# Performance work log

Hardware: AMD Instinct MI355X
Metric: run time of the kernel (lower is better)

The kernel has to match this reference:

```python
import jax, jax.numpy as jnp
import numpy as np

B, S, D = 2, 2048, 1024      # batch, seq, d_model
H, DH = 16, 64               # heads, head_dim
E, F, K = 16, 256, 2         # n_experts, expert_size, top_k


def setup_inputs() -> dict:
    key = jax.random.key(0)
    ks = jax.random.split(key, 12)
    w = lambda k, shape: (jax.random.normal(k, shape, jnp.float32) * 0.02)
    return {
        "hidden_states": jax.random.normal(ks[0], (B, S, D), jnp.float32),
        "Wq": w(ks[1], (D, D)),
        "Wk": w(ks[2], (D, D)),
        "Wv": w(ks[3], (D, D)),
        "Wo": w(ks[4], (D, D)),
        "ln1_scale": jnp.ones((D,), jnp.float32),
        "ln1_bias": jnp.zeros((D,), jnp.float32),
        "ln2_scale": jnp.ones((D,), jnp.float32),
        "ln2_bias": jnp.zeros((D,), jnp.float32),
        "W_sel": w(ks[5], (D, E)),
        "W1": w(ks[6], (E, D, F)),
        "W2": w(ks[7], (E, F, D)),
    }


def _layernorm(x, scale, bias, eps=1e-5):
    mu = jnp.mean(x, axis=-1, keepdims=True)
    var = jnp.mean(jnp.square(x - mu), axis=-1, keepdims=True)
    return (x - mu) * jax.lax.rsqrt(var + eps) * scale + bias


def reference(hidden_states, Wq, Wk, Wv, Wo, ln1_scale, ln1_bias,
              ln2_scale, ln2_bias, W_sel, W1, W2):
    x = hidden_states
    # ---- self-attention sublayer (pre-LN, residual) ----
    h = _layernorm(x, ln1_scale, ln1_bias)
    q = (h @ Wq).reshape(B, S, H, DH)
    k = (h @ Wk).reshape(B, S, H, DH)
    v = (h @ Wv).reshape(B, S, H, DH)
    scores = jnp.einsum("bqhd,bkhd->bhqk", q, k) / np.float32(np.sqrt(DH))
    attn = jax.nn.softmax(scores, axis=-1)
    ctx = jnp.einsum("bhqk,bkhd->bqhd", attn, v).reshape(B, S, D)
    x = x + ctx @ Wo

    # ---- SigmaMoE FFN sublayer (pre-LN, residual) ----
    h = _layernorm(x, ln2_scale, ln2_bias).reshape(B * S, D)  # [T, D]
    sel = jax.nn.sigmoid(h @ W_sel)                            # [T, E]
    vals, idx = jax.lax.top_k(sel, K)                          # [T, K]
    T = B * S
    gates = jnp.zeros((T, E), h.dtype).at[jnp.arange(T)[:, None], idx].set(vals)
    # expert MLPs, gate applied to each expert's output
    up = jax.nn.relu(jnp.einsum("td,edf->tef", h, W1))         # [T, E, F]
    up = up * gates[:, :, None]
    moe_out = jnp.einsum("tef,efd->td", up, W2).reshape(B, S, D)
    return x + moe_out
```

## Files before the change

kernel.cpp:

```cpp
#include <hip/hip_runtime.h>

typedef unsigned short u16;
typedef __attribute__((ext_vector_type(8))) short s16x8;
typedef __attribute__((ext_vector_type(4))) float f32x4;

typedef __attribute__((address_space(3))) unsigned int lds_u32_t;
typedef __attribute__((address_space(1))) unsigned int glb_u32_t;

__device__ __forceinline__ float bf2f(u16 u) {
    union { unsigned int i; float f; } c; c.i = ((unsigned int)u) << 16; return c.f;
}
__device__ __forceinline__ u16 f2bf(float f) {
    union { float f; unsigned int u; } c; c.f = f;
    unsigned int u = c.u;
    unsigned int r = (u + 0x7fffu + ((u >> 16) & 1u)) >> 16;
    return (u16)r;
}
__device__ __forceinline__ void glds16(const u16* g, short* l) {
    __builtin_amdgcn_global_load_lds((glb_u32_t*)g, (lds_u32_t*)l, 16, 0, 0);
}

__global__ __launch_bounds__(256) void transpose_split_kernel(const float* __restrict__ src,
                                                              u16* __restrict__ dh,
                                                              u16* __restrict__ dl,
                                                              int R, int C) {
    __shared__ float tile[32][33];
    int c0 = blockIdx.x * 32, r0 = blockIdx.y * 32;
    int tx = threadIdx.x & 31, ty = threadIdx.x >> 5;
    for (int i = 0; i < 4; i++)
        tile[ty + 8 * i][tx] = src[(size_t)(r0 + ty + 8 * i) * C + c0 + tx];
    __syncthreads();
    for (int i = 0; i < 4; i++) {
        float v = tile[tx][ty + 8 * i];
        u16 hb = f2bf(v);
        size_t idx = (size_t)(c0 + ty + 8 * i) * R + r0 + tx;
        dh[idx] = hb;
        dl[idx] = f2bf(v - bf2f(hb));
    }
}

__global__ __launch_bounds__(256) void transpose_f2b_kernel(const float* __restrict__ src,
                                                            u16* __restrict__ dst,
                                                            int R, int C) {
    __shared__ float tile[32][33];
    size_t zoff = (size_t)blockIdx.z * R * C;
    int c0 = blockIdx.x * 32, r0 = blockIdx.y * 32;
    int tx = threadIdx.x & 31, ty = threadIdx.x >> 5;
    for (int i = 0; i < 4; i++)
        tile[ty + 8 * i][tx] = src[zoff + (size_t)(r0 + ty + 8 * i) * C + c0 + tx];
    __syncthreads();
    for (int i = 0; i < 4; i++)
        dst[zoff + (size_t)(c0 + ty + 8 * i) * R + r0 + tx] = f2bf(tile[tx][ty + 8 * i]);
}

__global__ __launch_bounds__(256) void ln_split_kernel(const float* __restrict__ x,
                                                       const float* __restrict__ sc,
                                                       const float* __restrict__ bi,
                                                       u16* __restrict__ oh,
                                                       u16* __restrict__ ol) {
    int row = blockIdx.x, tid = threadIdx.x;
    f32x4 u = *(const f32x4*)(x + (size_t)row * 1024 + tid * 4);
    float s = u[0] + u[1] + u[2] + u[3];
    float ss = u[0]*u[0] + u[1]*u[1] + u[2]*u[2] + u[3]*u[3];
    for (int off = 1; off < 64; off <<= 1) { s += __shfl_xor(s, off, 64); ss += __shfl_xor(ss, off, 64); }
    __shared__ float red[8];
    if ((tid & 63) == 0) { red[tid >> 6] = s; red[4 + (tid >> 6)] = ss; }
    __syncthreads();
    s = red[0] + red[1] + red[2] + red[3];
    ss = red[4] + red[5] + red[6] + red[7];
    float mu = s * (1.0f / 1024.0f);
    float rstd = rsqrtf(ss * (1.0f / 1024.0f) - mu * mu + 1e-5f);
    f32x4 g = *(const f32x4*)(sc + tid * 4);
    f32x4 b = *(const f32x4*)(bi + tid * 4);
    size_t o = (size_t)row * 1024 + tid * 4;
    for (int i = 0; i < 4; i++) {
        float v = (u[i] - mu) * rstd * g[i] + b[i];
        u16 hb = f2bf(v);
        oh[o + i] = hb;
        ol[o + i] = f2bf(v - bf2f(hb));
    }
}

__global__ __launch_bounds__(256) void ln_f2b_kernel(const float* __restrict__ x,
                                                     const float* __restrict__ sc,
                                                     const float* __restrict__ bi,
                                                     u16* __restrict__ out) {
    int row = blockIdx.x, tid = threadIdx.x;
    f32x4 u = *(const f32x4*)(x + (size_t)row * 1024 + tid * 4);
    float s = u[0] + u[1] + u[2] + u[3];
    float ss = u[0]*u[0] + u[1]*u[1] + u[2]*u[2] + u[3]*u[3];
    for (int off = 1; off < 64; off <<= 1) { s += __shfl_xor(s, off, 64); ss += __shfl_xor(ss, off, 64); }
    __shared__ float red[8];
    if ((tid & 63) == 0) { red[tid >> 6] = s; red[4 + (tid >> 6)] = ss; }
    __syncthreads();
    s = red[0] + red[1] + red[2] + red[3];
    ss = red[4] + red[5] + red[6] + red[7];
    float mu = s * (1.0f / 1024.0f);
    float rstd = rsqrtf(ss * (1.0f / 1024.0f) - mu * mu + 1e-5f);
    f32x4 g = *(const f32x4*)(sc + tid * 4);
    f32x4 b = *(const f32x4*)(bi + tid * 4);
    u16* op = out + (size_t)row * 1024 + tid * 4;
    for (int i = 0; i < 4; i++)
        op[i] = f2bf((u[i] - mu) * rstd * g[i] + b[i]);
}

__global__ __launch_bounds__(256) void gemm3_qkv(const u16* __restrict__ Ah_g,
                                                 const u16* __restrict__ Al_g,
                                                 const u16* __restrict__ Bh_g,
                                                 const u16* __restrict__ Bl_g,
                                                 u16* __restrict__ Ch, u16* __restrict__ Cl,
                                                 float scale) {
    const int K = 1024;
    __shared__ __align__(16) short Ahs[128 * 32], Als[128 * 32];
    __shared__ __align__(16) short Bhs[128 * 32], Bls[128 * 32];
    int m0 = blockIdx.y * 128, n0 = blockIdx.x * 128;
    int tid = threadIdx.x, lane = tid & 63, w = tid >> 6;
    int wm = (w & 1) * 64, wn = (w >> 1) * 64;
    int lr = lane & 15, lq = lane >> 4;
    int r0 = w * 32 + (lane >> 2);
    int cv = (lane & 3) * 8;
    const u16* pAh = Ah_g + (size_t)(m0 + r0) * K + cv;
    const u16* pAl = Al_g + (size_t)(m0 + r0) * K + cv;
    const u16* pBh = Bh_g + (size_t)(n0 + r0) * K + cv;
    const u16* pBl = Bl_g + (size_t)(n0 + r0) * K + cv;
    size_t st16 = (size_t)16 * K;
    f32x4 acc[4][4] = {};

    for (int k0 = 0; k0 < K; k0 += 32) {
        glds16(pAh + k0, &Ahs[w * 1024]);  glds16(pAh + k0 + st16, &Ahs[w * 1024 + 512]);
        glds16(pAl + k0, &Als[w * 1024]);  glds16(pAl + k0 + st16, &Als[w * 1024 + 512]);
        glds16(pBh + k0, &Bhs[w * 1024]);  glds16(pBh + k0 + st16, &Bhs[w * 1024 + 512]);
        glds16(pBl + k0, &Bls[w * 1024]);  glds16(pBl + k0 + st16, &Bls[w * 1024 + 512]);
        __syncthreads();
        s16x8 ah[4], al[4], bh[4], bl[4];
        #pragma unroll
        for (int i = 0; i < 4; i++) {
            int off = (wm + i * 16 + lr) * 32 + lq * 8;
            ah[i] = *(const s16x8*)&Ahs[off];
            al[i] = *(const s16x8*)&Als[off];
        }
        #pragma unroll
        for (int j = 0; j < 4; j++) {
            int off = (wn + j * 16 + lr) * 32 + lq * 8;
            bh[j] = *(const s16x8*)&Bhs[off];
            bl[j] = *(const s16x8*)&Bls[off];
        }
        #pragma unroll
        for (int i = 0; i < 4; i++)
            #pragma unroll
            for (int j = 0; j < 4; j++) {
                acc[i][j] = __builtin_amdgcn_mfma_f32_16x16x32_bf16(al[i], bh[j], acc[i][j], 0, 0, 0);
                acc[i][j] = __builtin_amdgcn_mfma_f32_16x16x32_bf16(ah[i], bl[j], acc[i][j], 0, 0, 0);
                acc[i][j] = __builtin_amdgcn_mfma_f32_16x16x32_bf16(ah[i], bh[j], acc[i][j], 0, 0, 0);
            }
        __syncthreads();
    }

    int seg = n0 >> 10;
    float sc = (seg == 0) ? scale : 1.0f;
    u16* Chp = Ch + (size_t)seg * 8388608;
    u16* Clp = Cl + (size_t)seg * 8388608;
    int c0 = (n0 & 1023) + wn;
    #pragma unroll
    for (int i = 0; i < 4; i++)
        #pragma unroll
        for (int j = 0; j < 4; j++)
            #pragma unroll
            for (int r = 0; r < 4; r++) {
                int row = m0 + wm + i * 16 + lq * 4 + r;
                int col = c0 + j * 16 + lr;
                float vv = acc[i][j][r] * sc;
                u16 hb = f2bf(vv);
                u16 lb = f2bf(vv - bf2f(hb));
                size_t idx = (size_t)row * 1024 + col;
                Chp[idx] = hb; Clp[idx] = lb;
            }
}

__global__ __launch_bounds__(256) void gemm3_res(const u16* __restrict__ Ah_g,
                                                 const u16* __restrict__ Al_g,
                                                 const u16* __restrict__ Bh_g,
                                                 const u16* __restrict__ Bl_g,
                                                 float* __restrict__ C,
                                                 const float* __restrict__ res) {
    const int K = 1024, N = 1024;
    __shared__ __align__(16) short Ahs[128 * 32], Als[128 * 32];
    __shared__ __align__(16) short Bhs[128 * 32], Bls[128 * 32];
    int m0 = blockIdx.y * 128, n0 = blockIdx.x * 128;
    int tid = threadIdx.x, lane = tid & 63, w = tid >> 6;
    int wm = (w & 1) * 64, wn = (w >> 1) * 64;
    int lr = lane & 15, lq = lane >> 4;
    int r0 = w * 32 + (lane >> 2);
    int cv = (lane & 3) * 8;
    const u16* pAh = Ah_g + (size_t)(m0 + r0) * K + cv;
    const u16* pAl = Al_g + (size_t)(m0 + r0) * K + cv;
    const u16* pBh = Bh_g + (size_t)(n0 + r0) * K + cv;
    const u16* pBl = Bl_g + (size_t)(n0 + r0) * K + cv;
    size_t st16 = (size_t)16 * K;
    f32x4 acc[4][4] = {};

    for (int k0 = 0; k0 < K; k0 += 32) {
        glds16(pAh + k0, &Ahs[w * 1024]);  glds16(pAh + k0 + st16, &Ahs[w * 1024 + 512]);
        glds16(pAl + k0, &Als[w * 1024]);  glds16(pAl + k0 + st16, &Als[w * 1024 + 512]);
        glds16(pBh + k0, &Bhs[w * 1024]);  glds16(pBh + k0 + st16, &Bhs[w * 1024 + 512]);
        glds16(pBl + k0, &Bls[w * 1024]);  glds16(pBl + k0 + st16, &Bls[w * 1024 + 512]);
        __syncthreads();
        s16x8 ah[4], al[4], bh[4], bl[4];
        #pragma unroll
        for (int i = 0; i < 4; i++) {
            int off = (wm + i * 16 + lr) * 32 + lq * 8;
            ah[i] = *(const s16x8*)&Ahs[off];
            al[i] = *(const s16x8*)&Als[off];
        }
        #pragma unroll
        for (int j = 0; j < 4; j++) {
            int off = (wn + j * 16 + lr) * 32 + lq * 8;
            bh[j] = *(const s16x8*)&Bhs[off];
            bl[j] = *(const s16x8*)&Bls[off];
        }
        #pragma unroll
        for (int i = 0; i < 4; i++)
            #pragma unroll
            for (int j = 0; j < 4; j++) {
                acc[i][j] = __builtin_amdgcn_mfma_f32_16x16x32_bf16(al[i], bh[j], acc[i][j], 0, 0, 0);
                acc[i][j] = __builtin_amdgcn_mfma_f32_16x16x32_bf16(ah[i], bl[j], acc[i][j], 0, 0, 0);
                acc[i][j] = __builtin_amdgcn_mfma_f32_16x16x32_bf16(ah[i], bh[j], acc[i][j], 0, 0, 0);
            }
        __syncthreads();
    }

    #pragma unroll
    for (int i = 0; i < 4; i++)
        #pragma unroll
        for (int j = 0; j < 4; j++)
            #pragma unroll
            for (int r = 0; r < 4; r++) {
                int row = m0 + wm + i * 16 + lq * 4 + r;
                int col = n0 + wn + j * 16 + lr;
                size_t idx = (size_t)row * N + col;
                C[idx] = acc[i][j][r] + res[idx];
            }
}

__global__ __launch_bounds__(256) void gemm_moe_up(const u16* __restrict__ A,
                                                   const u16* __restrict__ BT,
                                                   u16* __restrict__ C,
                                                   const float* __restrict__ gates) {
    const int K = 1024, N = 4096;
    __shared__ __align__(16) short As[128 * 32];
    __shared__ __align__(16) short Bs[128 * 32];
    int m0 = blockIdx.y * 128, n0 = blockIdx.x * 128;
    int tid = threadIdx.x, lane = tid & 63, w = tid >> 6;
    int wm = (w & 1) * 64, wn = (w >> 1) * 64;
    int lr = lane & 15, lq = lane >> 4;
    int r0 = w * 32 + (lane >> 2);
    int cv = (lane & 3) * 8;
    const u16* pA = A  + (size_t)(m0 + r0) * K + cv;
    const u16* pB = BT + (size_t)(n0 + r0) * K + cv;
    size_t st16 = (size_t)16 * K;
    f32x4 acc[4][4] = {};

    for (int k0 = 0; k0 < K; k0 += 32) {
        glds16(pA + k0, &As[w * 1024]);  glds16(pA + k0 + st16, &As[w * 1024 + 512]);
        glds16(pB + k0, &Bs[w * 1024]);  glds16(pB + k0 + st16, &Bs[w * 1024 + 512]);
        __syncthreads();
        s16x8 av[4], bv[4];
        #pragma unroll
        for (int i = 0; i < 4; i++) av[i] = *(const s16x8*)&As[(wm + i * 16 + lr) * 32 + lq * 8];
        #pragma unroll
        for (int j = 0; j < 4; j++) bv[j] = *(const s16x8*)&Bs[(wn + j * 16 + lr) * 32 + lq * 8];
        #pragma unroll
        for (int i = 0; i < 4; i++)
            #pragma unroll
            for (int j = 0; j < 4; j++)
                acc[i][j] = __builtin_amdgcn_mfma_f32_16x16x32_bf16(av[i], bv[j], acc[i][j], 0, 0, 0);
        __syncthreads();
    }

    #pragma unroll
    for (int i = 0; i < 4; i++)
        #pragma unroll
        for (int j = 0; j < 4; j++)
            #pragma unroll
            for (int r = 0; r < 4; r++) {
                int row = m0 + wm + i * 16 + lq * 4 + r;
                int col = n0 + wn + j * 16 + lr;
                float g = gates[(size_t)row * 16 + (col >> 8)];
                C[(size_t)row * N + col] = f2bf(fmaxf(acc[i][j][r], 0.0f) * g);
            }
}

__global__ __launch_bounds__(256) void gemm_moe_down(const u16* __restrict__ A,
                                                     const u16* __restrict__ BT,
                                                     float* __restrict__ C,
                                                     const float* __restrict__ res) {
    const int K = 4096, N = 1024;
    __shared__ __align__(16) short As[128 * 32];
    __shared__ __align__(16) short Bs[128 * 32];
    int m0 = blockIdx.y * 128, n0 = blockIdx.x * 128;
    int tid = threadIdx.x, lane = tid & 63, w = tid >> 6;
    int wm = (w & 1) * 64, wn = (w >> 1) * 64;
    int lr = lane & 15, lq = lane >> 4;
    int r0 = w * 32 + (lane >> 2);
    int cv = (lane & 3) * 8;
    const u16* pA = A  + (size_t)(m0 + r0) * K + cv;
    const u16* pB = BT + (size_t)(n0 + r0) * K + cv;
    size_t st16 = (size_t)16 * K;
    f32x4 acc[4][4] = {};

    for (int k0 = 0; k0 < K; k0 += 32) {
        glds16(pA + k0, &As[w * 1024]);  glds16(pA + k0 + st16, &As[w * 1024 + 512]);
        glds16(pB + k0, &Bs[w * 1024]);  glds16(pB + k0 + st16, &Bs[w * 1024 + 512]);
        __syncthreads();
        s16x8 av[4], bv[4];
        #pragma unroll
        for (int i = 0; i < 4; i++) av[i] = *(const s16x8*)&As[(wm + i * 16 + lr) * 32 + lq * 8];
        #pragma unroll
        for (int j = 0; j < 4; j++) bv[j] = *(const s16x8*)&Bs[(wn + j * 16 + lr) * 32 + lq * 8];
        #pragma unroll
        for (int i = 0; i < 4; i++)
            #pragma unroll
            for (int j = 0; j < 4; j++)
                acc[i][j] = __builtin_amdgcn_mfma_f32_16x16x32_bf16(av[i], bv[j], acc[i][j], 0, 0, 0);
        __syncthreads();
    }

    #pragma unroll
    for (int i = 0; i < 4; i++)
        #pragma unroll
        for (int j = 0; j < 4; j++)
            #pragma unroll
            for (int r = 0; r < 4; r++) {
                int row = m0 + wm + i * 16 + lq * 4 + r;
                int col = n0 + wn + j * 16 + lr;
                size_t idx = (size_t)row * N + col;
                C[idx] = acc[i][j][r] + res[idx];
            }
}

__global__ __launch_bounds__(256) void vtrans_kernel(const u16* __restrict__ v_hi,
                                                     const u16* __restrict__ v_lo,
                                                     u16* __restrict__ vT_hi,
                                                     u16* __restrict__ vT_lo) {
    __shared__ __align__(16) short tile[64][72];
    int st = blockIdx.x, bh = blockIdx.y;
    int b = bh >> 4, h = bh & 15;
    int tid = threadIdx.x;
    int i = tid >> 2, seg = (tid & 3) * 16;
    for (int p = 0; p < 2; p++) {
        const u16* src = p ? v_lo : v_hi;
        u16* dst = p ? vT_lo : vT_hi;
        size_t goff = (size_t)(b * 2048 + st * 64 + i) * 1024 + h * 64 + seg;
        *(s16x8*)&tile[i][seg]     = *(const s16x8*)&src[goff];
        *(s16x8*)&tile[i][seg + 8] = *(const s16x8*)&src[goff + 8];
        __syncthreads();
        s16x8 o0, o1;
        for (int j = 0; j < 8; j++) { o0[j] = tile[seg + j][i]; o1[j] = tile[seg + 8 + j][i]; }
        size_t doff = ((size_t)bh * 64 + i) * 2048 + st * 64 + seg;
        *(s16x8*)&dst[doff]     = o0;
        *(s16x8*)&dst[doff + 8] = o1;
        __syncthreads();
    }
}

__global__ __launch_bounds__(256) void attn_mfma(const u16* __restrict__ qh_g,
                                                 const u16* __restrict__ ql_g,
                                                 const u16* __restrict__ kh_g,
                                                 const u16* __restrict__ kl_g,
                                                 const u16* __restrict__ vth_g,
                                                 const u16* __restrict__ vtl_g,
                                                 u16* __restrict__ ch_g,
                                                 u16* __restrict__ cl_g) {
    __shared__ __align__(16) short Ksh[64][72], Ksl[64][72], Vsh[64][72], Vsl[64][72];
    __shared__ __align__(16) short Ph[4][16 * 64], Pl[4][16 * 64];
    int lin = blockIdx.x + 16 * blockIdx.y;
    int xcd = lin & 7, rest = lin >> 3;
    int qt = rest & 15;
    int bh = xcd + 8 * (rest >> 4);
    int b = bh >> 4, h = bh & 15;
    int tid = threadIdx.x, w = tid >> 6, lane = tid & 63;
    int lr = lane & 15, lq = lane >> 4;
    int qbase = qt * 128 + w * 32;

    s16x8 qfh[2][2], qfl[2][2];
    for (int rt = 0; rt < 2; rt++)
        for (int kc = 0; kc < 2; kc++) {
            size_t qoff = (size_t)(b * 2048 + qbase + rt * 16 + lr) * 1024 + h * 64 + kc * 32 + lq * 8;
            qfh[rt][kc] = *(const s16x8*)&qh_g[qoff];
            qfl[rt][kc] = *(const s16x8*)&ql_g[qoff];
        }

    float m_[2][4], l_[2][4];
    f32x4 O[2][4] = {};
    for (int rt = 0; rt < 2; rt++)
        for (int r = 0; r < 4; r++) { m_[rt][r] = -1e30f; l_[rt][r] = 0.0f; }

    for (int kc0 = 0; kc0 < 2048; kc0 += 64) {
        {
            int kk = tid >> 2, seg = (tid & 3) * 16;
            size_t goff = (size_t)(b * 2048 + kc0 + kk) * 1024 + h * 64 + seg;
            *(s16x8*)&Ksh[kk][seg]     = *(const s16x8*)&kh_g[goff];
            *(s16x8*)&Ksh[kk][seg + 8] = *(const s16x8*)&kh_g[goff + 8];
            *(s16x8*)&Ksl[kk][seg]     = *(const s16x8*)&kl_g[goff];
            *(s16x8*)&Ksl[kk][seg + 8] = *(const s16x8*)&kl_g[goff + 8];
            size_t voff = ((size_t)bh * 64 + kk) * 2048 + kc0 + seg;
            *(s16x8*)&Vsh[kk][seg]     = *(const s16x8*)&vth_g[voff];
            *(s16x8*)&Vsh[kk][seg + 8] = *(const s16x8*)&vth_g[voff + 8];
            *(s16x8*)&Vsl[kk][seg]     = *(const s16x8*)&vtl_g[voff];
            *(s16x8*)&Vsl[kk][seg + 8] = *(const s16x8*)&vtl_g[voff + 8];
        }
        __syncthreads();

        f32x4 s[2][4] = {};
        for (int ct = 0; ct < 4; ct++)
            for (int kc = 0; kc < 2; kc++) {
                s16x8 kbh = *(const s16x8*)&Ksh[ct * 16 + lr][kc * 32 + lq * 8];
                s16x8 kbl = *(const s16x8*)&Ksl[ct * 16 + lr][kc * 32 + lq * 8];
                for (int rt = 0; rt < 2; rt++) {
                    s[rt][ct] = __builtin_amdgcn_mfma_f32_16x16x32_bf16(qfl[rt][kc], kbh, s[rt][ct], 0, 0, 0);
                    s[rt][ct] = __builtin_amdgcn_mfma_f32_16x16x32_bf16(qfh[rt][kc], kbl, s[rt][ct], 0, 0, 0);
                    s[rt][ct] = __builtin_amdgcn_mfma_f32_16x16x32_bf16(qfh[rt][kc], kbh, s[rt][ct], 0, 0, 0);
                }
            }

        for (int rt = 0; rt < 2; rt++) {
            float al[4];
            for (int ri = 0; ri < 4; ri++) {
                float mx = fmaxf(fmaxf(s[rt][0][ri], s[rt][1][ri]), fmaxf(s[rt][2][ri], s[rt][3][ri]));
                for (int off = 1; off < 16; off <<= 1) mx = fmaxf(mx, __shfl_xor(mx, off, 64));
                float mn = fmaxf(m_[rt][ri], mx);
                float a = __expf(m_[rt][ri] - mn);
                m_[rt][ri] = mn; al[ri] = a;
                float ps = 0.0f;
                for (int ct = 0; ct < 4; ct++) {
                    float p = __expf(s[rt][ct][ri] - mn);
                    s[rt][ct][ri] = p; ps += p;
                }
                for (int off = 1; off < 16; off <<= 1) ps += __shfl_xor(ps, off, 64);
                l_[rt][ri] = l_[rt][ri] * a + ps;
            }
            for (int nt = 0; nt < 4; nt++)
                for (int ri = 0; ri < 4; ri++) O[rt][nt][ri] *= al[ri];
            for (int ct = 0; ct < 4; ct++)
                for (int ri = 0; ri < 4; ri++) {
                    float p = s[rt][ct][ri];
                    u16 hb = f2bf(p);
                    u16 lb = f2bf(p - bf2f(hb));
                    int row = lq * 4 + ri, col = ct * 16 + lr;
                    int pidx = (row * 64 + col) ^ ((row & 7) << 3);
                    Ph[w][pidx] = (short)hb;
                    Pl[w][pidx] = (short)lb;
                }
            asm volatile("s_waitcnt lgkmcnt(0)" ::: "memory");
            __builtin_amdgcn_sched_barrier(0);
            __builtin_amdgcn_s_setprio(1);
            for (int kc = 0; kc < 2; kc++) {
                int pidx = (lr * 64 + kc * 32 + lq * 8) ^ ((lr & 7) << 3);
                s16x8 pah = *(const s16x8*)&Ph[w][pidx];
                s16x8 pal = *(const s16x8*)&Pl[w][pidx];
                for (int nt = 0; nt < 4; nt++) {
                    s16x8 vbh = *(const s16x8*)&Vsh[nt * 16 + lr][kc * 32 + lq * 8];
                    s16x8 vbl = *(const s16x8*)&Vsl[nt * 16 + lr][kc * 32 + lq * 8];
                    O[rt][nt] = __builtin_amdgcn_mfma_f32_16x16x32_bf16(pal, vbh, O[rt][nt], 0, 0, 0);
                    O[rt][nt] = __builtin_amdgcn_mfma_f32_16x16x32_bf16(pah, vbl, O[rt][nt], 0, 0, 0);
                    O[rt][nt] = __builtin_amdgcn_mfma_f32_16x16x32_bf16(pah, vbh, O[rt][nt], 0, 0, 0);
                }
            }
            __builtin_amdgcn_s_setprio(0);
            asm volatile("s_waitcnt lgkmcnt(0)" ::: "memory");
            __builtin_amdgcn_sched_barrier(0);
        }
        __syncthreads();
    }

    for (int rt = 0; rt < 2; rt++)
        for (int nt = 0; nt < 4; nt++)
            for (int ri = 0; ri < 4; ri++) {
                int row = qbase + rt * 16 + lq * 4 + ri;
                int d = nt * 16 + lr;
                float v = O[rt][nt][ri] / l_[rt][ri];
                u16 hb = f2bf(v);
                size_t idx = (size_t)(b * 2048 + row) * 1024 + h * 64 + d;
                ch_g[idx] = hb;
                cl_g[idx] = f2bf(v - bf2f(hb));
            }
}

__global__ __launch_bounds__(256) void router_kernel(const float* __restrict__ x2,
                                                     const float* __restrict__ sc,
                                                     const float* __restrict__ bi,
                                                     const float* __restrict__ Wsel,
                                                     float* __restrict__ gates) {
    int tid = threadIdx.x, w = tid >> 6, lane = tid & 63;
    int t = blockIdx.x * 4 + w;
    const float* xp = x2 + (size_t)t * 1024;
    float s = 0.0f, ss = 0.0f;
    for (int i = 0; i < 16; i++) {
        float v = xp[lane * 16 + i];
        s += v; ss += v * v;
    }
    for (int off = 1; off < 64; off <<= 1) { s += __shfl_xor(s, off, 64); ss += __shfl_xor(ss, off, 64); }
    float mu = s * (1.0f / 1024.0f);
    float rstd = rsqrtf(ss * (1.0f / 1024.0f) - mu * mu + 1e-5f);
    int e = lane & 15, part = lane >> 4;
    float acc = 0.0f;
    for (int d = part * 256; d < part * 256 + 256; d++) {
        float h = (xp[d] - mu) * rstd * sc[d] + bi[d];
        acc += h * Wsel[(size_t)d * 16 + e];
    }
    acc += __shfl_xor(acc, 16, 64);
    acc += __shfl_xor(acc, 32, 64);
    float v = 1.0f / (1.0f + __expf(-acc));
    float m1 = v;
    for (int off = 1; off < 64; off <<= 1) m1 = fmaxf(m1, __shfl_xor(m1, off, 64));
    unsigned long long b1 = __ballot(v == m1);
    int e1 = (__ffsll(b1) - 1) & 15;
    float v2 = (e == e1) ? -1e30f : v;
    float m2 = v2;
    for (int off = 1; off < 64; off <<= 1) m2 = fmaxf(m2, __shfl_xor(m2, off, 64));
    unsigned long long b2 = __ballot(v2 == m2);
    int e2 = (__ffsll(b2) - 1) & 15;
    if (lane < 16)
        gates[(size_t)t * 16 + e] = (e == e1) ? m1 : (e == e2 ? m2 : 0.0f);
}

extern "C" void kernel_launch(void* const* d_in, const int* in_sizes, int n_in,
                              void* d_out, int out_size, void* d_ws, size_t ws_size,
                              hipStream_t stream) {
    const float* x    = (const float*)d_in[0];
    const float* Wq   = (const float*)d_in[1];
    const float* Wk   = (const float*)d_in[2];
    const float* Wv   = (const float*)d_in[3];
    const float* Wo   = (const float*)d_in[4];
    const float* ln1s = (const float*)d_in[5];
    const float* ln1b = (const float*)d_in[6];
    const float* ln2s = (const float*)d_in[7];
    const float* ln2b = (const float*)d_in[8];
    const float* Wsel = (const float*)d_in[9];
    const float* W1   = (const float*)d_in[10];
    const float* W2   = (const float*)d_in[11];
    float* out = (float*)d_out;

    char* ws = (char*)d_ws;
    const size_t MB = 1024 * 1024;
    u16*   h1_h  = (u16*)  (ws + 0 * MB);
    u16*   h1_l  = (u16*)  (ws + 8 * MB);
    u16*   vT_hi = (u16*)  (ws + 0 * MB);
    u16*   vT_lo = (u16*)  (ws + 8 * MB);
    u16*   h2    = (u16*)  (ws + 0 * MB);
    float* gates = (float*)(ws + 8 * MB);
    u16*   q_hi  = (u16*)  (ws + 16 * MB);
    u16*   q_lo  = (u16*)  (ws + 24 * MB);
    u16*   k_hi  = (u16*)  (ws + 32 * MB);
    u16*   k_lo  = (u16*)  (ws + 40 * MB);
    u16*   up    = (u16*)  (ws + 16 * MB);
    u16*   v_hi  = (u16*)  (ws + 48 * MB);
    u16*   v_lo  = (u16*)  (ws + 56 * MB);
    u16*   ctx_h = (u16*)  (ws + 48 * MB);
    u16*   ctx_l = (u16*)  (ws + 56 * MB);
    float* x2    = (float*)(ws + 64 * MB);
    u16*   WqT_h = (u16*)  (ws + 80 * MB);
    u16*   WkT_h = (u16*)  (ws + 82 * MB);
    u16*   WvT_h = (u16*)  (ws + 84 * MB);
    u16*   WqT_l = (u16*)  (ws + 86 * MB);
    u16*   WkT_l = (u16*)  (ws + 88 * MB);
    u16*   WvT_l = (u16*)  (ws + 90 * MB);
    u16*   WoT_h = (u16*)  (ws + 92 * MB);
    u16*   WoT_l = (u16*)  (ws + 94 * MB);
    u16*   W1T   = (u16*)  (ws + 80 * MB);
    u16*   W2T   = (u16*)  (ws + 88 * MB);

    transpose_split_kernel<<<dim3(32, 32), 256, 0, stream>>>(Wq, WqT_h, WqT_l, 1024, 1024);
    transpose_split_kernel<<<dim3(32, 32), 256, 0, stream>>>(Wk, WkT_h, WkT_l, 1024, 1024);
    transpose_split_kernel<<<dim3(32, 32), 256, 0, stream>>>(Wv, WvT_h, WvT_l, 1024, 1024);
    transpose_split_kernel<<<dim3(32, 32), 256, 0, stream>>>(Wo, WoT_h, WoT_l, 1024, 1024);

    ln_split_kernel<<<4096, 256, 0, stream>>>(x, ln1s, ln1b, h1_h, h1_l);
    gemm3_qkv<<<dim3(24, 32), 256, 0, stream>>>(h1_h, h1_l, WqT_h, WqT_l, q_hi, q_lo, 0.125f);
    vtrans_kernel<<<dim3(32, 32), 256, 0, stream>>>(v_hi, v_lo, vT_hi, vT_lo);
    attn_mfma<<<dim3(16, 32), 256, 0, stream>>>(q_hi, q_lo, k_hi, k_lo, vT_hi, vT_lo, ctx_h, ctx_l);
    gemm3_res<<<dim3(8, 32), 256, 0, stream>>>(ctx_h, ctx_l, WoT_h, WoT_l, x2, x);
    ln_f2b_kernel<<<4096, 256, 0, stream>>>(x2, ln2s, ln2b, h2);
    router_kernel<<<1024, 256, 0, stream>>>(x2, ln2s, ln2b, Wsel, gates);
    transpose_f2b_kernel<<<dim3(8, 32, 16), 256, 0, stream>>>(W1, W1T, 1024, 256);
    transpose_f2b_kernel<<<dim3(32, 128, 1), 256, 0, stream>>>(W2, W2T, 4096, 1024);
    gemm_moe_up<<<dim3(32, 32), 256, 0, stream>>>(h2, W1T, up, gates);
    gemm_moe_down<<<dim3(8, 32), 256, 0, stream>>>(up, W2T, out, x2);
}
```

Measured before the change: 638.7 us.

## Route MoE tokens to experts and compute only selected expert GEMMs

The router now builds per-expert token lists with atomic counters. The up and down GEMMs gather only the tokens routed to each expert instead of running dense over all 16 experts. The down projection scatter-adds into the output with float atomics after an init kernel copies in the residual. This removes about 8x of the MoE FLOPs, but output summation order becomes nondeterministic and the grid assumes at most 80 row tiles.

```diff
diff --git a/kernel.cpp b/kernel.cpp
--- a/kernel.cpp
+++ b/kernel.cpp
@@ -242,27 +242,50 @@
             }
 }
 
-__global__ __launch_bounds__(256) void gemm_moe_up(const u16* __restrict__ A,
-                                                   const u16* __restrict__ BT,
-                                                   u16* __restrict__ C,
-                                                   const float* __restrict__ gates) {
-    const int K = 1024, N = 4096;
+__global__ __launch_bounds__(256) void init_out_kernel(const float* __restrict__ x2,
+                                                       float* __restrict__ out) {
+    size_t i = ((size_t)blockIdx.x * 256 + threadIdx.x) * 4;
+    *(f32x4*)(out + i) = *(const f32x4*)(x2 + i);
+}
+
+__global__ __launch_bounds__(256) void gemm_moe_up_sparse(const u16* __restrict__ h2,
+                                                          const u16* __restrict__ W1T,
+                                                          const int* __restrict__ cnt,
+                                                          const int* __restrict__ list,
+                                                          const float* __restrict__ gates,
+                                                          u16* __restrict__ up_buf) {
+    const int K = 1024;
     __shared__ __align__(16) short As[128 * 32];
     __shared__ __align__(16) short Bs[128 * 32];
-    int m0 = blockIdx.y * 128, n0 = blockIdx.x * 128;
+    int e = -1, tstart = 0;
+    {
+        int ty = blockIdx.y, at = 0;
+        for (int i = 0; i < 16; i++) {
+            int nt = (cnt[i] + 127) >> 7;
+            if (ty < at + nt) { e = i; tstart = (ty - at) * 128; break; }
+            at += nt;
+        }
+    }
+    if (e < 0) return;
+    int ncnt = cnt[e];
+    int n0 = blockIdx.x * 128;
     int tid = threadIdx.x, lane = tid & 63, w = tid >> 6;
     int wm = (w & 1) * 64, wn = (w >> 1) * 64;
     int lr = lane & 15, lq = lane >> 4;
     int r0 = w * 32 + (lane >> 2);
     int cv = (lane & 3) * 8;
-    const u16* pA = A  + (size_t)(m0 + r0) * K + cv;
-    const u16* pB = BT + (size_t)(n0 + r0) * K + cv;
+    int p0 = tstart + r0, p1 = tstart + r0 + 16;
+    int t0 = list[e * 4096 + (p0 < ncnt ? p0 : ncnt - 1)];
+    int t1 = list[e * 4096 + (p1 < ncnt ? p1 : ncnt - 1)];
+    const u16* pA0 = h2 + (size_t)t0 * K + cv;
+    const u16* pA1 = h2 + (size_t)t1 * K + cv;
+    const u16* pB  = W1T + (size_t)(e * 256 + n0 + r0) * K + cv;
     size_t st16 = (size_t)16 * K;
     f32x4 acc[4][4] = {};
 
     for (int k0 = 0; k0 < K; k0 += 32) {
-        glds16(pA + k0, &As[w * 1024]);  glds16(pA + k0 + st16, &As[w * 1024 + 512]);
-        glds16(pB + k0, &Bs[w * 1024]);  glds16(pB + k0 + st16, &Bs[w * 1024 + 512]);
+        glds16(pA0 + k0, &As[w * 1024]);  glds16(pA1 + k0, &As[w * 1024 + 512]);
+        glds16(pB + k0, &Bs[w * 1024]);   glds16(pB + k0 + st16, &Bs[w * 1024 + 512]);
         __syncthreads();
         s16x8 av[4], bv[4];
         #pragma unroll
@@ -283,34 +306,54 @@
         for (int j = 0; j < 4; j++)
             #pragma unroll
             for (int r = 0; r < 4; r++) {
-                int row = m0 + wm + i * 16 + lq * 4 + r;
-                int col = n0 + wn + j * 16 + lr;
-                float g = gates[(size_t)row * 16 + (col >> 8)];
-                C[(size_t)row * N + col] = f2bf(fmaxf(acc[i][j][r], 0.0f) * g);
-            }
-}
-
-__global__ __launch_bounds__(256) void gemm_moe_down(const u16* __restrict__ A,
-                                                     const u16* __restrict__ BT,
-                                                     float* __restrict__ C,
-                                                     const float* __restrict__ res) {
-    const int K = 4096, N = 1024;
+                int rl = wm + i * 16 + lq * 4 + r;
+                int p = tstart + rl;
+                if (p < ncnt) {
+                    int t = list[e * 4096 + p];
+                    float g = gates[(size_t)t * 16 + e];
+                    int col = n0 + wn + j * 16 + lr;
+                    up_buf[(size_t)(e * 4096 + p) * 256 + col] = f2bf(fmaxf(acc[i][j][r], 0.0f) * g);
+                }
+            }
+}
+
+__global__ __launch_bounds__(256) void gemm_moe_down_sparse(const u16* __restrict__ up_buf,
+                                                            const u16* __restrict__ W2T,
+                                                            const int* __restrict__ cnt,
+                                                            const int* __restrict__ list,
+                                                            float* __restrict__ out) {
+    const int K = 256;
     __shared__ __align__(16) short As[128 * 32];
     __shared__ __align__(16) short Bs[128 * 32];
-    int m0 = blockIdx.y * 128, n0 = blockIdx.x * 128;
+    int e = -1, tstart = 0;
+    {
+        int ty = blockIdx.y, at = 0;
+        for (int i = 0; i < 16; i++) {
+            int nt = (cnt[i] + 127) >> 7;
+            if (ty < at + nt) { e = i; tstart = (ty - at) * 128; break; }
+            at += nt;
+        }
+    }
+    if (e < 0) return;
+    int ncnt = cnt[e];
+    int n0 = blockIdx.x * 128;
     int tid = threadIdx.x, lane = tid & 63, w = tid >> 6;
     int wm = (w & 1) * 64, wn = (w >> 1) * 64;
     int lr = lane & 15, lq = lane >> 4;
     int r0 = w * 32 + (lane >> 2);
     int cv = (lane & 3) * 8;
-    const u16* pA = A  + (size_t)(m0 + r0) * K + cv;
-    const u16* pB = BT + (size_t)(n0 + r0) * K + cv;
-    size_t st16 = (size_t)16 * K;
+    int p0 = tstart + r0, p1 = tstart + r0 + 16;
+    int pc0 = p0 < ncnt ? p0 : ncnt - 1;
+    int pc1 = p1 < ncnt ? p1 : ncnt - 1;
+    const u16* pA0 = up_buf + (size_t)(e * 4096 + pc0) * 256 + cv;
+    const u16* pA1 = up_buf + (size_t)(e * 4096 + pc1) * 256 + cv;
+    const u16* pB  = W2T + (size_t)(n0 + r0) * 4096 + e * 256 + cv;
+    size_t st16 = (size_t)16 * 4096;
     f32x4 acc[4][4] = {};
 
     for (int k0 = 0; k0 < K; k0 += 32) {
-        glds16(pA + k0, &As[w * 1024]);  glds16(pA + k0 + st16, &As[w * 1024 + 512]);
-        glds16(pB + k0, &Bs[w * 1024]);  glds16(pB + k0 + st16, &Bs[w * 1024 + 512]);
+        glds16(pA0 + k0, &As[w * 1024]);  glds16(pA1 + k0, &As[w * 1024 + 512]);
+        glds16(pB + k0, &Bs[w * 1024]);   glds16(pB + k0 + st16, &Bs[w * 1024 + 512]);
         __syncthreads();
         s16x8 av[4], bv[4];
         #pragma unroll
@@ -331,10 +374,13 @@
         for (int j = 0; j < 4; j++)
             #pragma unroll
             for (int r = 0; r < 4; r++) {
-                int row = m0 + wm + i * 16 + lq * 4 + r;
-                int col = n0 + wn + j * 16 + lr;
-                size_t idx = (size_t)row * N + col;
-                C[idx] = acc[i][j][r] + res[idx];
+                int rl = wm + i * 16 + lq * 4 + r;
+                int p = tstart + rl;
+                if (p < ncnt) {
+                    int t = list[e * 4096 + p];
+                    int col = n0 + wn + j * 16 + lr;
+                    atomicAdd(&out[(size_t)t * 1024 + col], acc[i][j][r]);
+                }
             }
 }
 
@@ -490,7 +536,9 @@
                                                      const float* __restrict__ sc,
                                                      const float* __restrict__ bi,
                                                      const float* __restrict__ Wsel,
-                                                     float* __restrict__ gates) {
+                                                     float* __restrict__ gates,
+                                                     int* __restrict__ cnt,
+                                                     int* __restrict__ list) {
     int tid = threadIdx.x, w = tid >> 6, lane = tid & 63;
     int t = blockIdx.x * 4 + w;
     const float* xp = x2 + (size_t)t * 1024;
@@ -522,6 +570,12 @@
     int e2 = (__ffsll(b2) - 1) & 15;
     if (lane < 16)
         gates[(size_t)t * 16 + e] = (e == e1) ? m1 : (e == e2 ? m2 : 0.0f);
+    if (lane == 0) {
+        int p1 = atomicAdd(&cnt[e1], 1);
+        list[e1 * 4096 + p1] = t;
+        int p2 = atomicAdd(&cnt[e2], 1);
+        list[e2 * 4096 + p2] = t;
+    }
 }
 
 extern "C" void kernel_launch(void* const* d_in, const int* in_sizes, int n_in,
@@ -549,6 +603,8 @@
     u16*   vT_lo = (u16*)  (ws + 8 * MB);
     u16*   h2    = (u16*)  (ws + 0 * MB);
     float* gates = (float*)(ws + 8 * MB);
+    int*   cnt   = (int*)  (ws + 9 * MB);
+    int*   list  = (int*)  (ws + 9 * MB + 4096);
     u16*   q_hi  = (u16*)  (ws + 16 * MB);
     u16*   q_lo  = (u16*)  (ws + 24 * MB);
     u16*   k_hi  = (u16*)  (ws + 32 * MB);
@@ -581,9 +637,11 @@
     attn_mfma<<<dim3(16, 32), 256, 0, stream>>>(q_hi, q_lo, k_hi, k_lo, vT_hi, vT_lo, ctx_h, ctx_l);
     gemm3_res<<<dim3(8, 32), 256, 0, stream>>>(ctx_h, ctx_l, WoT_h, WoT_l, x2, x);
     ln_f2b_kernel<<<4096, 256, 0, stream>>>(x2, ln2s, ln2b, h2);
-    router_kernel<<<1024, 256, 0, stream>>>(x2, ln2s, ln2b, Wsel, gates);
+    hipMemsetAsync(cnt, 0, 16 * sizeof(int), stream);
+    router_kernel<<<1024, 256, 0, stream>>>(x2, ln2s, ln2b, Wsel, gates, cnt, list);
+    init_out_kernel<<<4096, 256, 0, stream>>>(x2, out);
     transpose_f2b_kernel<<<dim3(8, 32, 16), 256, 0, stream>>>(W1, W1T, 1024, 256);
     transpose_f2b_kernel<<<dim3(32, 128, 1), 256, 0, stream>>>(W2, W2T, 4096, 1024);
-    gemm_moe_up<<<dim3(32, 32), 256, 0, stream>>>(h2, W1T, up, gates);
-    gemm_moe_down<<<dim3(8, 32), 256, 0, stream>>>(up, W2T, out, x2);
-}
+    gemm_moe_up_sparse<<<dim3(2, 80), 256, 0, stream>>>(h2, W1T, cnt, list, gates, up);
+    gemm_moe_down_sparse<<<dim3(8, 80), 256, 0, stream>>>(up, W2T, cnt, list, out);
+}
```

After: 683.2 us. 1.07x slower.
